# Kernel optimization log

Measured on AMD Instinct MI355X. Metric: run time of the kernel, lower is better.

## Reference

```python
import jax, jax.numpy as jnp
import numpy as np
from jax import lax

B, T = 16, 128
H, FD = 24, 4          # H hours, FD fourier harmonics
L = 64                 # latent_dim
D = 256                # d_model
NH = 8                 # heads
C = 1 + H * FD         # cont_dim = 97
EPS = 1e-5


def setup_inputs() -> dict:
    key = jax.random.key(0)
    ks = jax.random.split(key, 32)
    r = lambda k, sh, s: (jax.random.normal(k, sh, dtype=jnp.float32) * s)
    z = lambda sh: jnp.zeros(sh, dtype=jnp.float32)
    o = lambda sh: jnp.ones(sh, dtype=jnp.float32)
    return {
        'x_cont': jax.random.normal(ks[0], (B, T, C), dtype=jnp.float32),
        'z0': z((1, 1, L)),                       # learned initial hidden state
        'W_ih': r(ks[1], (L, 1), 0.1),            # RNN input weights
        'W_hh': r(ks[2], (L, L), 0.1),            # RNN recurrent weights
        'b_ih': z((L,)),
        'b_hh': z((L,)),
        'Uf': r(ks[3], (H, FD), 0.01),            # fourier coefficients
        'Wfp': r(ks[4], (L, H), 0.05),            # fourier_proj (L != H)
        'bfp': z((L,)),
        'feat_embed': r(ks[5], (L, D), 0.02),
        'W_in': r(ks[6], (3 * D, D), 0.02),       # MHA in_proj
        'b_in': z((3 * D,)),
        'W_ao': r(ks[7], (D, D), 0.02),           # MHA out_proj
        'b_ao': z((D,)),
        'g1': o((D,)), 'be1': z((D,)),            # ln1
        'W1': r(ks[8], (4 * D, D), 0.02), 'b1': z((4 * D,)),
        'W2': r(ks[9], (D, 4 * D), 0.02), 'b2': z((D,)),
        'g2': o((D,)), 'be2': z((D,)),            # ln2
        'Wop': r(ks[10], (1, D), 0.02), 'bop': z((1,)),   # out_proj d_model->1
        'Wg': r(ks[11], (L, L), 0.05), 'bg': z((L,)),     # gate
        'A': r(ks[12], (H, L), 0.01),
        'c': z((H,)),
    }


def _ln(x, g, b):
    mu = jnp.mean(x, -1, keepdims=True)
    var = jnp.mean(jnp.square(x - mu), -1, keepdims=True)
    return (x - mu) * lax.rsqrt(var + EPS) * g + b


def reference(x_cont, z0, W_ih, W_hh, b_ih, b_hh, Uf, Wfp, bfp, feat_embed,
              W_in, b_in, W_ao, b_ao, g1, be1, W1, b1, W2, b2, g2, be2,
              Wop, bop, Wg, bg, A, c):
    Bb, Tt, Cc = x_cont.shape
    x0 = x_cont[:, :, :1]              # (B,T,1)
    xf = x_cont[:, :, 1:]              # (B,T,H*FD)

    # --- single-layer relu RNN over time ---
    h0 = jnp.broadcast_to(z0[0, 0], (Bb, L))

    def step(h, x_t):                  # x_t: (B,1)
        h = jax.nn.relu(x_t @ W_ih.T + b_ih + h @ W_hh.T + b_hh)
        return h, h

    _, hs = lax.scan(step, h0, jnp.swapaxes(x0, 0, 1))
    h = jnp.swapaxes(hs, 0, 1)         # (B,T,L)

    # --- fourier features ---
    xf_mat = xf.reshape(Bb, Tt, H, FD)
    fourier_h = jnp.einsum('bthf,hf->bth', xf_mat, Uf)   # (B,T,H)
    z = h + fourier_h @ Wfp.T + bfp                      # (B,T,L)

    # --- feature attention: tokens (B*T, L, D) ---
    N = Bb * Tt
    zf = z.reshape(N, L)
    tokens = zf[:, :, None] * feat_embed[None]           # (N,L,D)

    qkv = tokens @ W_in.T + b_in                         # (N,L,3D)
    q, k, v = jnp.split(qkv, 3, axis=-1)
    dh = D // NH
    split_heads = lambda t: t.reshape(N, L, NH, dh).transpose(0, 2, 1, 3)
    q, k, v = split_heads(q), split_heads(k), split_heads(v)
    att = jax.nn.softmax(jnp.einsum('nhqd,nhkd->nhqk', q, k) / np.sqrt(dh), axis=-1)
    ao = jnp.einsum('nhqk,nhkd->nhqd', att, v).transpose(0, 2, 1, 3).reshape(N, L, D)
    ao = ao @ W_ao.T + b_ao

    t1 = _ln(tokens + ao, g1, be1)
    ffn = jax.nn.relu(t1 @ W1.T + b1) @ W2.T + b2
    t2 = _ln(t1 + ffn, g2, be2)
    delta = (t2 @ Wop.T + bop)[..., 0].reshape(Bb, Tt, L)

    gate = jax.nn.sigmoid(z @ Wg.T + bg)
    z_out = z + gate * delta

    o = z_out @ A.T + c                                  # (B,T,H)
    return (o, z_out)
```

## Files before the change

kernel.cpp:

```cpp
#include <hip/hip_runtime.h>

typedef short bf16x8 __attribute__((ext_vector_type(8)));
typedef float f32x4  __attribute__((ext_vector_type(4)));

__device__ __forceinline__ unsigned short f2b(float f){
  union { float f; unsigned u; } v; v.f = f;
  unsigned r = v.u + 0x7FFFu + ((v.u >> 16) & 1u);
  return (unsigned short)(r >> 16);
}
__device__ __forceinline__ float b2f(unsigned short s){
  union { unsigned u; float f; } v; v.u = ((unsigned)s) << 16;
  return v.f;
}
__device__ __forceinline__ unsigned pk2(float lo, float hi){
  unsigned r;
  asm("v_cvt_pk_bf16_f32 %0, %1, %2" : "=v"(r) : "v"(lo), "v"(hi));
  return r;
}

__global__ void k_pre_qkv(const float* __restrict__ FE, const float* __restrict__ W_in,
                          float* __restrict__ Qm, float* __restrict__ Km, float* __restrict__ Vm){
  int id = blockIdx.x*256 + threadIdx.x;
  int part = id >> 14;
  int l = (id >> 8) & 63;
  int d = id & 255;
  const float4* fe = (const float4*)(FE + l*256);
  const float4* wr = (const float4*)(W_in + (part*256 + d)*256);
  float s = 0.f;
  #pragma unroll 8
  for (int k=0;k<64;k++){
    float4 a = fe[k], b = wr[k];
    s += a.x*b.x + a.y*b.y + a.z*b.z + a.w*b.w;
  }
  float* dst = (part==0)?Qm:((part==1)?Km:Vm);
  dst[l*256+d] = s;
}

__global__ void k_pre2(const float* __restrict__ Qm, const float* __restrict__ Km,
                       const float* __restrict__ Vm,
                       const float* __restrict__ b_in, const float* __restrict__ W_ao,
                       const float* __restrict__ b_ao, const float* __restrict__ FE,
                       float* __restrict__ Gc, float* __restrict__ U,
                       float* __restrict__ W, float* __restrict__ S,
                       float* __restrict__ abias, short* __restrict__ M2c,
                       const float* __restrict__ W1, const float* __restrict__ W2,
                       short* __restrict__ W1c, short* __restrict__ W2c,
                       float* __restrict__ FEc,
                       const float* __restrict__ x_cont, const float* __restrict__ z0,
                       const float* __restrict__ W_ih, const float* __restrict__ W_hh,
                       const float* __restrict__ b_ih, const float* __restrict__ b_hh,
                       const float* __restrict__ Uf, const float* __restrict__ Wfp,
                       const float* __restrict__ bfp, float* __restrict__ zout){
  int bid = blockIdx.x;
  int tid = threadIdx.x;
  if (bid < 198){
    int id = bid*256 + tid;
    const float inv = 0.17677669529663687f;
    if (id < 32768){
      int h = id >> 12, ks = (id>>11)&1, w4 = (id>>9)&3, lane = (id>>3)&63, j = id&7;
      int lq = w4*16 + (lane&15);
      int lk = ks*32 + (lane>>4)*8 + j;
      const float* qp = Qm + lq*256 + h*32;
      const float* kp = Km + lk*256 + h*32;
      float s=0.f;
      #pragma unroll
      for (int d=0;d<32;d++) s += qp[d]*kp[d];
      Gc[id] = s*inv;
    } else if (id < 33280){
      int j = id - 32768; int h = j>>6, lq = j&63;
      const float* qp = Qm + lq*256 + h*32;
      const float* bk = b_in + 256 + h*32;
      float s=0.f;
      #pragma unroll
      for (int d=0;d<32;d++) s += qp[d]*bk[d];
      U[j] = s*inv;
    } else if (id < 33792){
      int j = id - 33280; int h = j>>6, lk = j&63;
      const float* kp = Km + lk*256 + h*32;
      const float* bq = b_in + h*32;
      float s=0.f;
      #pragma unroll
      for (int d=0;d<32;d++) s += bq[d]*kp[d];
      W[j] = s*inv;
    } else if (id < 33800){
      int h = id - 33792;
      float s=0.f;
      #pragma unroll
      for (int d=0;d<32;d++) s += b_in[h*32+d]*b_in[256+h*32+d];
      S[h] = s*inv;
    } else if (id < 34056){
      int e = id - 33800;
      float s = b_ao[e];
      for (int d=0; d<256; d++) s += b_in[512+d]*W_ao[e*256+d];
      abias[e] = s;
    } else if (id < 50440){
      int o = id - 34056;
      int tt = o>>12, et = (o>>10)&3, w4 = (o>>8)&3, lane = (o>>2)&63, j = o&3;
      int row = tt*16 + (lane&15);
      int col = w4*64 + et*16 + (lane>>4)*4 + j;
      FEc[o] = FE[row*256 + col];
    }
    return;
  }
  if (bid < 710){
    int o = (bid-198)*256 + tid;
    int h = o>>14, ks = (o>>13)&1, w4 = (o>>11)&3, et = (o>>9)&3, lane = (o>>3)&63, j = o&7;
    int e = w4*64 + et*16 + (lane&15);
    int lk = ks*32 + (lane>>4)*8 + j;
    const float* vp = Vm + lk*256 + h*32;
    const float* wp = W_ao + e*256 + h*32;
    float s=0.f;
    #pragma unroll
    for (int d=0;d<32;d++) s += vp[d]*wp[d];
    M2c[o] = (short)f2b(s);
    return;
  }
  if (bid < 2758){
    int id3 = (bid-710)*256 + tid;
    if (id3 < 262144){
      int o = id3;
      int c = o>>15, ks = (o>>12)&7, w4 = (o>>10)&3, ct = (o>>9)&1, lane = (o>>3)&63, j = o&7;
      int row = c*128 + w4*32 + ct*16 + (lane&15);
      int col = ks*32 + (lane>>4)*8 + j;
      W1c[o] = (short)f2b(W1[row*256 + col]);
    } else {
      int o = id3 - 262144;
      int c = o>>15, ks2 = (o>>13)&3, w4 = (o>>11)&3, et = (o>>9)&3, lane = (o>>3)&63, j = o&7;
      int row = w4*64 + et*16 + (lane&15);
      int col = c*128 + ks2*32 + (lane>>4)*8 + j;
      W2c[o] = (short)f2b(W2[row*1024 + col]);
    }
    return;
  }
  {
    int b = bid - 2758;
    int l = tid;
    bool act = (l < 64);
    __shared__ float h_sh[64];
    __shared__ float fh_sh[24];
    __shared__ float WfpT[24][64];
    float wr[64];
    float wih=0, bb=0, bf=0;
    float uf0=0,uf1=0,uf2=0,uf3=0;
    if (act){
      #pragma unroll
      for (int j=0;j<64;j++) wr[j] = W_hh[l*64+j];
      #pragma unroll
      for (int j=0;j<24;j++) WfpT[j][l] = Wfp[l*24+j];
      wih = W_ih[l];
      bb  = b_ih[l] + b_hh[l];
      bf  = bfp[l];
      if (l < 24){ uf0=Uf[l*4+0]; uf1=Uf[l*4+1]; uf2=Uf[l*4+2]; uf3=Uf[l*4+3]; }
      h_sh[l] = z0[l];
    }
    __syncthreads();
    const float* xb = x_cont + (size_t)b*128*97;
    for (int t=0;t<128;t++){
      float hn = 0.f, fh = 0.f;
      if (act){
        float x0 = xb[t*97];
        float a0=0,a1=0,a2=0,a3=0;
        #pragma unroll
        for (int j=0;j<64;j+=4){
          a0 += wr[j  ]*h_sh[j  ];
          a1 += wr[j+1]*h_sh[j+1];
          a2 += wr[j+2]*h_sh[j+2];
          a3 += wr[j+3]*h_sh[j+3];
        }
        hn = fmaxf(x0*wih + bb + ((a0+a1)+(a2+a3)), 0.f);
        if (l < 24){
          const float* xf = xb + t*97 + 1 + l*4;
          fh = xf[0]*uf0 + xf[1]*uf1 + xf[2]*uf2 + xf[3]*uf3;
        }
      }
      __syncthreads();
      if (act){
        h_sh[l] = hn;
        if (l < 24) fh_sh[l] = fh;
      }
      __syncthreads();
      if (act){
        float zv = hn + bf;
        #pragma unroll
        for (int j=0;j<24;j++) zv += fh_sh[j]*WfpT[j][l];
        zout[((size_t)b*128 + t)*64 + l] = zv;
      }
    }
  }
}

__global__ __launch_bounds__(256, 2) void k_main(
  const float* __restrict__ zall, const float* __restrict__ Gc,
  const float* __restrict__ Ubuf, const float* __restrict__ Wbuf, const float* __restrict__ Sbuf,
  const float* __restrict__ abias, const short* __restrict__ M2c,
  const float* __restrict__ FEc,
  const short* __restrict__ W1c, const float* __restrict__ b1,
  const short* __restrict__ W2c, const float* __restrict__ b2,
  const float* __restrict__ g1, const float* __restrict__ be1,
  const float* __restrict__ g2, const float* __restrict__ be2,
  const float* __restrict__ Wop, const float* __restrict__ bop,
  const float* __restrict__ Wg, const float* __restrict__ bg,
  const float* __restrict__ Amat, const float* __restrict__ cvec,
  float* __restrict__ out)
{
  const int n = blockIdx.x;
  const int tid = threadIdx.x;
  const int w = tid >> 6, lane = tid & 63, lg = lane >> 4, lr = lane & 15;
  const int cb = w * 64;

  __shared__ __align__(16) short t1_sh[64][264];
  __shared__ __align__(16) char  upoolA[17408];
  __shared__ __align__(16) char  upoolB[17408];
  __shared__ float redA[4][64];
  __shared__ float redB[4][64];
  __shared__ float z_sh[64];

  short (*midA)[136] = reinterpret_cast<short (*)[136]>(upoolA);
  short (*midB)[136] = reinterpret_cast<short (*)[136]>(upoolB);
  short (*pa_sh)[4][2][64][8] = reinterpret_cast<short (*)[4][2][64][8]>(upoolA);

  if (tid < 64) z_sh[tid] = zall[n*64 + tid];
  __syncthreads();

  float zkf[16];
  #pragma unroll
  for (int i=0;i<16;i++) zkf[i] = z_sh[(i>>3)*32 + lg*8 + (i&7)];

  f32x4 acc[4][4];
  #pragma unroll
  for (int et=0;et<4;et++)
    #pragma unroll
    for (int tt=0;tt<4;tt++){ f32x4 zz = {0.f,0.f,0.f,0.f}; acc[et][tt] = zz; }

  const int lq_own = w*16 + lr;
  const float zq_own = z_sh[lq_own];

  #pragma unroll 1
  for (int h=0; h<8; ++h){
    bf16x8 am[8];
    #pragma unroll
    for (int ks=0;ks<2;ks++)
      #pragma unroll
      for (int et=0;et<4;et++)
        am[ks*4+et] = *(const bf16x8*)(M2c + h*16384 + ks*8192 + w*2048 + et*512 + lane*8);
    {
      const float sh = Sbuf[h];
      const float uh = Ubuf[h*64 + lq_own];
      float e0[16];
      #pragma unroll
      for (int ks=0;ks<2;ks++){
        const float* gbase = Gc + h*4096 + ks*2048 + w*512 + lane*8;
        f32x4 ga = *(const f32x4*)(gbase);
        f32x4 gb = *(const f32x4*)(gbase + 4);
        f32x4 wa = *(const f32x4*)(Wbuf + h*64 + ks*32 + lg*8);
        f32x4 wb = *(const f32x4*)(Wbuf + h*64 + ks*32 + lg*8 + 4);
        #pragma unroll
        for (int j=0;j<4;j++){
          float zk = zkf[ks*8+j];
          e0[ks*8+j]   = zq_own*(zk*ga[j] + uh) + (zk*wa[j] + sh);
          float zk2 = zkf[ks*8+4+j];
          e0[ks*8+4+j] = zq_own*(zk2*gb[j] + uh) + (zk2*wb[j] + sh);
        }
      }
      float mx = e0[0];
      #pragma unroll
      for (int i=1;i<16;i++) mx = fmaxf(mx, e0[i]);
      mx = fmaxf(mx, __shfl_xor(mx,16));
      mx = fmaxf(mx, __shfl_xor(mx,32));
      float sum = 0.f;
      #pragma unroll
      for (int i=0;i<16;i++){ e0[i] = __expf(e0[i]-mx); sum += e0[i]; }
      sum += __shfl_xor(sum,16);
      sum += __shfl_xor(sum,32);
      float inv = 1.f/sum;
      #pragma unroll
      for (int ks=0;ks<2;ks++){
        union { bf16x8 v; unsigned u[4]; } pa;
        #pragma unroll
        for (int p=0;p<4;p++)
          pa.u[p] = pk2(e0[ks*8+2*p]*inv*zkf[ks*8+2*p], e0[ks*8+2*p+1]*inv*zkf[ks*8+2*p+1]);
        *(bf16x8*)&pa_sh[h&1][w][ks][lane][0] = pa.v;
      }
    }
    __syncthreads();
    __builtin_amdgcn_s_setprio(1);
    #pragma unroll
    for (int ks=0; ks<2; ks++){
      bf16x8 bt[4];
      #pragma unroll
      for (int tt=0;tt<4;tt++) bt[tt] = *(const bf16x8*)&pa_sh[h&1][tt][ks][lane][0];
      #pragma unroll
      for (int et=0;et<4;et++)
        #pragma unroll
        for (int tt=0;tt<4;tt++)
          acc[et][tt] = __builtin_amdgcn_mfma_f32_16x16x32_bf16(am[ks*4+et], bt[tt], acc[et][tt], 0,0,0);
    }
    __builtin_amdgcn_s_setprio(0);
  }

  f32x4 ab4[4], g14[4], be14[4];
  #pragma unroll
  for (int et=0;et<4;et++){
    int e0_ = cb + et*16 + lg*4;
    ab4[et]  = *(const f32x4*)(abias + e0_);
    g14[et]  = *(const f32x4*)(g1 + e0_);
    be14[et] = *(const f32x4*)(be1 + e0_);
  }
  float sum1[4], ssq1[4];
  #pragma unroll
  for (int tt=0;tt<4;tt++){
    int tok = tt*16 + lr;
    float zt = z_sh[tok];
    float s = 0.f, sq = 0.f;
    #pragma unroll
    for (int et=0;et<4;et++){
      f32x4 fe = *(const f32x4*)(FEc + tt*4096 + et*1024 + w*256 + lane*4);
      #pragma unroll
      for (int r=0;r<4;r++){
        float v = acc[et][tt][r] + ab4[et][r] + zt*fe[r];
        acc[et][tt][r] = v; s += v; sq += v*v;
      }
    }
    s  += __shfl_xor(s,16);  s  += __shfl_xor(s,32);
    sq += __shfl_xor(sq,16); sq += __shfl_xor(sq,32);
    sum1[tt] = s; ssq1[tt] = sq;
  }
  if (lane < 16){
    #pragma unroll
    for (int tt=0;tt<4;tt++){ redA[w][tt*16+lane] = sum1[tt]; redB[w][tt*16+lane] = ssq1[tt]; }
  }
  __syncthreads();
  float mu1[4], rs1[4];
  #pragma unroll
  for (int tt=0;tt<4;tt++){
    int tok = tt*16 + lr;
    float s  = redA[0][tok] + redA[1][tok] + redA[2][tok] + redA[3][tok];
    float sq = redB[0][tok] + redB[1][tok] + redB[2][tok] + redB[3][tok];
    float m = s * (1.f/256.f);
    mu1[tt] = m;
    rs1[tt] = rsqrtf(sq*(1.f/256.f) - m*m + 1e-5f);
  }
  #pragma unroll
  for (int et=0;et<4;et++)
    #pragma unroll
    for (int tt=0;tt<4;tt++){
      uint2 p;
      float v0 = (acc[et][tt][0]-mu1[tt])*rs1[tt]*g14[et][0] + be14[et][0];
      float v1 = (acc[et][tt][1]-mu1[tt])*rs1[tt]*g14[et][1] + be14[et][1];
      float v2 = (acc[et][tt][2]-mu1[tt])*rs1[tt]*g14[et][2] + be14[et][2];
      float v3 = (acc[et][tt][3]-mu1[tt])*rs1[tt]*g14[et][3] + be14[et][3];
      p.x = pk2(v0,v1); p.y = pk2(v2,v3);
      *(uint2*)&t1_sh[tt*16+lr][cb + et*16 + lg*4] = p;
    }
  __syncthreads();

  #pragma unroll
  for (int et=0;et<4;et++)
    #pragma unroll
    for (int tt=0;tt<4;tt++){ f32x4 zz = {0.f,0.f,0.f,0.f}; acc[et][tt] = zz; }

  #pragma unroll 1
  for (int c=0; c<8; c++){
    f32x4 midv[2][4];
    #pragma unroll
    for (int ct=0;ct<2;ct++){
      f32x4 bi = *(const f32x4*)(b1 + c*128 + w*32 + ct*16 + lg*4);
      #pragma unroll
      for (int tt=0;tt<4;tt++) midv[ct][tt] = bi;
    }
    bf16x8 aw2[16];
    #pragma unroll
    for (int ks2=0;ks2<2;ks2++)
      #pragma unroll
      for (int et=0;et<4;et++)
        aw2[ks2*4+et] = *(const bf16x8*)(W2c + c*32768 + ks2*8192 + w*2048 + et*512 + lane*8);
    #pragma unroll
    for (int ks=0; ks<4; ks++){
      bf16x8 bt[4], aw[2];
      #pragma unroll
      for (int tt=0;tt<4;tt++) bt[tt] = *(const bf16x8*)&t1_sh[tt*16+lr][ks*32 + lg*8];
      #pragma unroll
      for (int ct=0;ct<2;ct++)
        aw[ct] = *(const bf16x8*)(W1c + c*32768 + ks*4096 + w*1024 + ct*512 + lane*8);
      #pragma unroll
      for (int ct=0;ct<2;ct++)
        #pragma unroll
        for (int tt=0;tt<4;tt++)
          midv[ct][tt] = __builtin_amdgcn_mfma_f32_16x16x32_bf16(aw[ct], bt[tt], midv[ct][tt], 0,0,0);
    }
    #pragma unroll
    for (int ks2=2;ks2<4;ks2++)
      #pragma unroll
      for (int et=0;et<4;et++)
        aw2[ks2*4+et] = *(const bf16x8*)(W2c + c*32768 + ks2*8192 + w*2048 + et*512 + lane*8);
    #pragma unroll
    for (int ks=4; ks<8; ks++){
      bf16x8 bt[4], aw[2];
      #pragma unroll
      for (int tt=0;tt<4;tt++) bt[tt] = *(const bf16x8*)&t1_sh[tt*16+lr][ks*32 + lg*8];
      #pragma unroll
      for (int ct=0;ct<2;ct++)
        aw[ct] = *(const bf16x8*)(W1c + c*32768 + ks*4096 + w*1024 + ct*512 + lane*8);
      #pragma unroll
      for (int ct=0;ct<2;ct++)
        #pragma unroll
        for (int tt=0;tt<4;tt++)
          midv[ct][tt] = __builtin_amdgcn_mfma_f32_16x16x32_bf16(aw[ct], bt[tt], midv[ct][tt], 0,0,0);
    }
    short (*mids_)[136] = (c & 1) ? midB : midA;
    #pragma unroll
    for (int ct=0;ct<2;ct++)
      #pragma unroll
      for (int tt=0;tt<4;tt++){
        uint2 p;
        p.x = pk2(fmaxf(midv[ct][tt][0],0.f), fmaxf(midv[ct][tt][1],0.f));
        p.y = pk2(fmaxf(midv[ct][tt][2],0.f), fmaxf(midv[ct][tt][3],0.f));
        *(uint2*)&mids_[tt*16+lr][w*32 + ct*16 + lg*4] = p;
      }
    __syncthreads();
    __builtin_amdgcn_s_setprio(1);
    #pragma unroll
    for (int ks2=0; ks2<4; ks2++){
      bf16x8 bm[4];
      #pragma unroll
      for (int tt=0;tt<4;tt++) bm[tt] = *(const bf16x8*)&mids_[tt*16+lr][ks2*32 + lg*8];
      #pragma unroll
      for (int et=0;et<4;et++)
        #pragma unroll
        for (int tt=0;tt<4;tt++)
          acc[et][tt] = __builtin_amdgcn_mfma_f32_16x16x32_bf16(aw2[ks2*4+et], bm[tt], acc[et][tt], 0,0,0);
    }
    __builtin_amdgcn_s_setprio(0);
  }

  f32x4 b24[4], g24[4], be24[4], wop4[4];
  #pragma unroll
  for (int et=0;et<4;et++){
    int e0_ = cb + et*16 + lg*4;
    b24[et]  = *(const f32x4*)(b2 + e0_);
    g24[et]  = *(const f32x4*)(g2 + e0_);
    be24[et] = *(const f32x4*)(be2 + e0_);
    wop4[et] = *(const f32x4*)(Wop + e0_);
  }
  float sum2[4], ssq2[4];
  #pragma unroll
  for (int tt=0;tt<4;tt++){
    int tok = tt*16 + lr;
    float s = 0.f, sq = 0.f;
    #pragma unroll
    for (int et=0;et<4;et++){
      uint2 t1v = *(const uint2*)&t1_sh[tok][cb + et*16 + lg*4];
      #pragma unroll
      for (int r=0;r<4;r++){
        unsigned short hs = (unsigned short)((r&1) ? ((r<2?t1v.x:t1v.y)>>16) : ((r<2?t1v.x:t1v.y)&0xFFFF));
        float v = acc[et][tt][r] + b24[et][r] + b2f(hs);
        acc[et][tt][r] = v; s += v; sq += v*v;
      }
    }
    s  += __shfl_xor(s,16);  s  += __shfl_xor(s,32);
    sq += __shfl_xor(sq,16); sq += __shfl_xor(sq,32);
    sum2[tt] = s; ssq2[tt] = sq;
  }
  if (lane < 16){
    #pragma unroll
    for (int tt=0;tt<4;tt++){ redA[w][tt*16+lane] = sum2[tt]; redB[w][tt*16+lane] = ssq2[tt]; }
  }
  __syncthreads();

  float gate = 0.f;
  if (tid < 64){
    float gacc = bg[tid];
    const f32x4* wgr = (const f32x4*)(Wg + tid*64);
    #pragma unroll
    for (int j=0;j<16;j++){
      f32x4 wv = wgr[j];
      f32x4 zv = *(const f32x4*)(z_sh + j*4);
      gacc += wv[0]*zv[0] + wv[1]*zv[1] + wv[2]*zv[2] + wv[3]*zv[3];
    }
    gate = 1.f/(1.f + __expf(-gacc));
  }

  float dpart[4];
  #pragma unroll
  for (int tt=0;tt<4;tt++){
    int tok = tt*16 + lr;
    float s  = redA[0][tok] + redA[1][tok] + redA[2][tok] + redA[3][tok];
    float sq = redB[0][tok] + redB[1][tok] + redB[2][tok] + redB[3][tok];
    float m = s * (1.f/256.f);
    float rs = rsqrtf(sq*(1.f/256.f) - m*m + 1e-5f);
    float d = 0.f;
    #pragma unroll
    for (int et=0;et<4;et++)
      #pragma unroll
      for (int r=0;r<4;r++){
        float t2 = (acc[et][tt][r]-m)*rs*g24[et][r] + be24[et][r];
        d += t2*wop4[et][r];
      }
    d += __shfl_xor(d,16); d += __shfl_xor(d,32);
    dpart[tt] = d;
  }
  __syncthreads();
  if (lane < 16){
    #pragma unroll
    for (int tt=0;tt<4;tt++) redA[w][tt*16+lane] = dpart[tt];
  }
  __syncthreads();
  if (tid < 64){
    float delta = redA[0][tid]+redA[1][tid]+redA[2][tid]+redA[3][tid] + bop[0];
    float zo = z_sh[tid] + gate*delta;
    out[49152 + (size_t)n*64 + tid] = zo;
    z_sh[tid] = zo;
  }
  __syncthreads();
  if (tid < 24){
    const float* ar = Amat + tid*64;
    float s = cvec[tid];
    #pragma unroll
    for (int j=0;j<64;j++) s += z_sh[j]*ar[j];
    out[(size_t)n*24 + tid] = s;
  }
}

extern "C" void kernel_launch(void* const* d_in, const int* in_sizes, int n_in,
                              void* d_out, int out_size, void* d_ws, size_t ws_size,
                              hipStream_t stream) {
  const float* x_cont = (const float*)d_in[0];
  const float* z0    = (const float*)d_in[1];
  const float* W_ih  = (const float*)d_in[2];
  const float* W_hh  = (const float*)d_in[3];
  const float* b_ih  = (const float*)d_in[4];
  const float* b_hh  = (const float*)d_in[5];
  const float* Uf    = (const float*)d_in[6];
  const float* Wfp   = (const float*)d_in[7];
  const float* bfp   = (const float*)d_in[8];
  const float* FE    = (const float*)d_in[9];
  const float* W_in  = (const float*)d_in[10];
  const float* b_in  = (const float*)d_in[11];
  const float* W_ao  = (const float*)d_in[12];
  const float* b_ao  = (const float*)d_in[13];
  const float* g1    = (const float*)d_in[14];
  const float* be1   = (const float*)d_in[15];
  const float* W1    = (const float*)d_in[16];
  const float* b1    = (const float*)d_in[17];
  const float* W2    = (const float*)d_in[18];
  const float* b2    = (const float*)d_in[19];
  const float* g2    = (const float*)d_in[20];
  const float* be2   = (const float*)d_in[21];
  const float* Wop   = (const float*)d_in[22];
  const float* bop   = (const float*)d_in[23];
  const float* Wg    = (const float*)d_in[24];
  const float* bg    = (const float*)d_in[25];
  const float* Amat  = (const float*)d_in[26];
  const float* cvec  = (const float*)d_in[27];
  float* out = (float*)d_out;
  char* ws = (char*)d_ws;

  float* z    = (float*)(ws + 0);
  float* Qm   = (float*)(ws + 524288);
  float* Km   = (float*)(ws + 589824);
  float* Vm   = (float*)(ws + 655360);
  float* Gc   = (float*)(ws + 720896);
  float* U    = (float*)(ws + 851968);
  float* Wb   = (float*)(ws + 854016);
  float* S    = (float*)(ws + 856064);
  float* ab   = (float*)(ws + 856320);
  short* M2c  = (short*)(ws + 857344);
  short* W1c  = (short*)(ws + 1119488);
  short* W2c  = (short*)(ws + 1643776);
  float* FEc  = (float*)(ws + 2168064);

  hipLaunchKernelGGL(k_pre_qkv, dim3(192), dim3(256), 0, stream, FE, W_in, Qm, Km, Vm);
  hipLaunchKernelGGL(k_pre2, dim3(2774), dim3(256), 0, stream,
                     Qm, Km, Vm, b_in, W_ao, b_ao, FE, Gc, U, Wb, S, ab, M2c,
                     W1, W2, W1c, W2c, FEc,
                     x_cont, z0, W_ih, W_hh, b_ih, b_hh, Uf, Wfp, bfp, z);
  hipLaunchKernelGGL(k_main, dim3(2048), dim3(256), 0, stream, z, Gc, U, Wb, S, ab, M2c, FEc,
                     W1c, b1, W2c, b2, g1, be1, g2, be2, Wop, bop, Wg, bg, Amat, cvec, out);
}
```

Baseline: 336.6 us.

## Tile QKV precompute in shared memory, schedule RNN blocks first, coalesce weight reads

Rewrites the FE·W_inᵀ precompute as a shared-memory tiled GEMM in 12 blocks, with each thread accumulating 16 outputs instead of one thread per output doing a strided dot product. The sequential RNN blocks move to the front of the k_pre2 grid so the long serial recurrence starts first and can overlap the bulk work. The W1/W2 bf16 repack now reads source rows contiguously and scatters the writes, which coalesces the global loads. The tiled precompute uses only 12 blocks, which leaves most compute units idle during that kernel.

```diff
diff --git a/kernel.cpp b/kernel.cpp
--- a/kernel.cpp
+++ b/kernel.cpp
@@ -18,22 +18,36 @@
   return r;
 }
 
-__global__ void k_pre_qkv(const float* __restrict__ FE, const float* __restrict__ W_in,
+__global__ __launch_bounds__(256) void k_pre_qkv(const float* __restrict__ FE, const float* __restrict__ W_in,
                           float* __restrict__ Qm, float* __restrict__ Km, float* __restrict__ Vm){
-  int id = blockIdx.x*256 + threadIdx.x;
-  int part = id >> 14;
-  int l = (id >> 8) & 63;
-  int d = id & 255;
-  const float4* fe = (const float4*)(FE + l*256);
-  const float4* wr = (const float4*)(W_in + (part*256 + d)*256);
-  float s = 0.f;
-  #pragma unroll 8
-  for (int k=0;k<64;k++){
-    float4 a = fe[k], b = wr[k];
-    s += a.x*b.x + a.y*b.y + a.z*b.z + a.w*b.w;
+  const int part = blockIdx.x >> 2, db = blockIdx.x & 3;
+  const int tid = threadIdx.x;
+  const int l = tid & 63, dg = tid >> 6;
+  __shared__ float Wt[64][65];
+  __shared__ float Ft[64][65];
+  float acc[16];
+  #pragma unroll
+  for (int i=0;i<16;i++) acc[i]=0.f;
+  for (int kc=0;kc<4;kc++){
+    __syncthreads();
+    #pragma unroll
+    for (int t=0;t<16;t++){
+      int id = tid + t*256;
+      int r = id >> 6, kk = id & 63;
+      Wt[r][kk] = W_in[(size_t)(part*256 + db*64 + r)*256 + kc*64 + kk];
+      Ft[r][kk] = FE[(size_t)r*256 + kc*64 + kk];
+    }
+    __syncthreads();
+    #pragma unroll 8
+    for (int kk=0;kk<64;kk++){
+      float fv = Ft[l][kk];
+      #pragma unroll
+      for (int i=0;i<16;i++) acc[i] += fv * Wt[dg*16+i][kk];
+    }
   }
   float* dst = (part==0)?Qm:((part==1)?Km:Vm);
-  dst[l*256+d] = s;
+  #pragma unroll
+  for (int i=0;i<16;i++) dst[l*256 + db*64 + dg*16 + i] = acc[i];
 }
 
 __global__ void k_pre2(const float* __restrict__ Qm, const float* __restrict__ Km,
@@ -53,8 +67,64 @@
                        const float* __restrict__ bfp, float* __restrict__ zout){
   int bid = blockIdx.x;
   int tid = threadIdx.x;
-  if (bid < 198){
-    int id = bid*256 + tid;
+  if (bid < 16){
+    int b = bid;
+    int l = tid;
+    bool act = (l < 64);
+    __shared__ float h_sh[64];
+    __shared__ float fh_sh[24];
+    __shared__ float WfpT[24][64];
+    float wr[64];
+    float wih=0, bb=0, bf=0;
+    float uf0=0,uf1=0,uf2=0,uf3=0;
+    if (act){
+      #pragma unroll
+      for (int j=0;j<64;j++) wr[j] = W_hh[l*64+j];
+      #pragma unroll
+      for (int j=0;j<24;j++) WfpT[j][l] = Wfp[l*24+j];
+      wih = W_ih[l];
+      bb  = b_ih[l] + b_hh[l];
+      bf  = bfp[l];
+      if (l < 24){ uf0=Uf[l*4+0]; uf1=Uf[l*4+1]; uf2=Uf[l*4+2]; uf3=Uf[l*4+3]; }
+      h_sh[l] = z0[l];
+    }
+    __syncthreads();
+    const float* xb = x_cont + (size_t)b*128*97;
+    for (int t=0;t<128;t++){
+      float hn = 0.f, fh = 0.f;
+      if (act){
+        float x0 = xb[t*97];
+        float a0=0,a1=0,a2=0,a3=0;
+        #pragma unroll
+        for (int j=0;j<64;j+=4){
+          a0 += wr[j  ]*h_sh[j  ];
+          a1 += wr[j+1]*h_sh[j+1];
+          a2 += wr[j+2]*h_sh[j+2];
+          a3 += wr[j+3]*h_sh[j+3];
+        }
+        hn = fmaxf(x0*wih + bb + ((a0+a1)+(a2+a3)), 0.f);
+        if (l < 24){
+          const float* xf = xb + t*97 + 1 + l*4;
+          fh = xf[0]*uf0 + xf[1]*uf1 + xf[2]*uf2 + xf[3]*uf3;
+        }
+      }
+      __syncthreads();
+      if (act){
+        h_sh[l] = hn;
+        if (l < 24) fh_sh[l] = fh;
+      }
+      __syncthreads();
+      if (act){
+        float zv = hn + bf;
+        #pragma unroll
+        for (int j=0;j<24;j++) zv += fh_sh[j]*WfpT[j][l];
+        zout[((size_t)b*128 + t)*64 + l] = zv;
+      }
+    }
+    return;
+  }
+  if (bid < 214){
+    int id = (bid-16)*256 + tid;
     const float inv = 0.17677669529663687f;
     if (id < 32768){
       int h = id >> 12, ks = (id>>11)&1, w4 = (id>>9)&3, lane = (id>>3)&63, j = id&7;
@@ -102,8 +172,8 @@
     }
     return;
   }
-  if (bid < 710){
-    int o = (bid-198)*256 + tid;
+  if (bid < 726){
+    int o = (bid-214)*256 + tid;
     int h = o>>14, ks = (o>>13)&1, w4 = (o>>11)&3, et = (o>>9)&3, lane = (o>>3)&63, j = o&7;
     int e = w4*64 + et*16 + (lane&15);
     int lk = ks*32 + (lane>>4)*8 + j;
@@ -115,77 +185,23 @@
     M2c[o] = (short)f2b(s);
     return;
   }
-  if (bid < 2758){
-    int id3 = (bid-710)*256 + tid;
+  {
+    int id3 = (bid-726)*256 + tid;
     if (id3 < 262144){
-      int o = id3;
-      int c = o>>15, ks = (o>>12)&7, w4 = (o>>10)&3, ct = (o>>9)&1, lane = (o>>3)&63, j = o&7;
-      int row = c*128 + w4*32 + ct*16 + (lane&15);
-      int col = ks*32 + (lane>>4)*8 + j;
-      W1c[o] = (short)f2b(W1[row*256 + col]);
+      int row = id3 >> 8, col = id3 & 255;
+      int c = row >> 7, w4 = (row>>5)&3, ct = (row>>4)&1, lrow = row & 15;
+      int ks = col >> 5, lhi = (col>>3)&3, j = col & 7;
+      int o = c*32768 + ks*4096 + w4*1024 + ct*512 + (lhi*16+lrow)*8 + j;
+      W1c[o] = (short)f2b(W1[id3]);
     } else {
-      int o = id3 - 262144;
-      int c = o>>15, ks2 = (o>>13)&3, w4 = (o>>11)&3, et = (o>>9)&3, lane = (o>>3)&63, j = o&7;
-      int row = w4*64 + et*16 + (lane&15);
-      int col = c*128 + ks2*32 + (lane>>4)*8 + j;
-      W2c[o] = (short)f2b(W2[row*1024 + col]);
+      int idx = id3 - 262144;
+      int row = idx >> 10, col = idx & 1023;
+      int w4 = row >> 6, et = (row>>4)&3, lrow = row & 15;
+      int c = col >> 7, ks2 = (col>>5)&3, lhi = (col>>3)&3, j = col & 7;
+      int o = c*32768 + ks2*8192 + w4*2048 + et*512 + (lhi*16+lrow)*8 + j;
+      W2c[o] = (short)f2b(W2[idx]);
     }
     return;
-  }
-  {
-    int b = bid - 2758;
-    int l = tid;
-    bool act = (l < 64);
-    __shared__ float h_sh[64];
-    __shared__ float fh_sh[24];
-    __shared__ float WfpT[24][64];
-    float wr[64];
-    float wih=0, bb=0, bf=0;
-    float uf0=0,uf1=0,uf2=0,uf3=0;
-    if (act){
-      #pragma unroll
-      for (int j=0;j<64;j++) wr[j] = W_hh[l*64+j];
-      #pragma unroll
-      for (int j=0;j<24;j++) WfpT[j][l] = Wfp[l*24+j];
-      wih = W_ih[l];
-      bb  = b_ih[l] + b_hh[l];
-      bf  = bfp[l];
-      if (l < 24){ uf0=Uf[l*4+0]; uf1=Uf[l*4+1]; uf2=Uf[l*4+2]; uf3=Uf[l*4+3]; }
-      h_sh[l] = z0[l];
-    }
-    __syncthreads();
-    const float* xb = x_cont + (size_t)b*128*97;
-    for (int t=0;t<128;t++){
-      float hn = 0.f, fh = 0.f;
-      if (act){
-        float x0 = xb[t*97];
-        float a0=0,a1=0,a2=0,a3=0;
-        #pragma unroll
-        for (int j=0;j<64;j+=4){
-          a0 += wr[j  ]*h_sh[j  ];
-          a1 += wr[j+1]*h_sh[j+1];
-          a2 += wr[j+2]*h_sh[j+2];
-          a3 += wr[j+3]*h_sh[j+3];
-        }
-        hn = fmaxf(x0*wih + bb + ((a0+a1)+(a2+a3)), 0.f);
-        if (l < 24){
-          const float* xf = xb + t*97 + 1 + l*4;
-          fh = xf[0]*uf0 + xf[1]*uf1 + xf[2]*uf2 + xf[3]*uf3;
-        }
-      }
-      __syncthreads();
-      if (act){
-        h_sh[l] = hn;
-        if (l < 24) fh_sh[l] = fh;
-      }
-      __syncthreads();
-      if (act){
-        float zv = hn + bf;
-        #pragma unroll
-        for (int j=0;j<24;j++) zv += fh_sh[j]*WfpT[j][l];
-        zout[((size_t)b*128 + t)*64 + l] = zv;
-      }
-    }
   }
 }
 
@@ -569,7 +585,7 @@
   short* W2c  = (short*)(ws + 1643776);
   float* FEc  = (float*)(ws + 2168064);
 
-  hipLaunchKernelGGL(k_pre_qkv, dim3(192), dim3(256), 0, stream, FE, W_in, Qm, Km, Vm);
+  hipLaunchKernelGGL(k_pre_qkv, dim3(12), dim3(256), 0, stream, FE, W_in, Qm, Km, Vm);
   hipLaunchKernelGGL(k_pre2, dim3(2774), dim3(256), 0, stream,
                      Qm, Km, Vm, b_in, W_ao, b_ao, FE, Gc, U, Wb, S, ab, M2c,
                      W1, W2, W1c, W2c, FEc,
```

Result: slower. 358.4 us (+6.5%).

## Raise k_main occupancy to three blocks, move RNN blocks first, coalesce weight repack

Applied to the files above, without the earlier changes.

k_main's launch bounds go from two to three blocks per CU. To fit, the double-buffered FFN mid buffer becomes a single buffer guarded by an extra barrier, and the M2c/W2 fragments are loaded just before use instead of prefetched into registers. In the prep kernel, the serial RNN blocks now take the lowest block indices so they start first, and the W1/W2 bf16 repack reads its source coalesced and scatters the writes. The trade is less latency hiding and an extra sync per chunk in exchange for more resident waves.

```diff
diff --git a/kernel.cpp b/kernel.cpp
--- a/kernel.cpp
+++ b/kernel.cpp
@@ -53,8 +53,64 @@
                        const float* __restrict__ bfp, float* __restrict__ zout){
   int bid = blockIdx.x;
   int tid = threadIdx.x;
-  if (bid < 198){
-    int id = bid*256 + tid;
+  if (bid < 16){
+    int b = bid;
+    int l = tid;
+    bool act = (l < 64);
+    __shared__ float h_sh[64];
+    __shared__ float fh_sh[24];
+    __shared__ float WfpT[24][64];
+    float wr[64];
+    float wih=0, bb=0, bf=0;
+    float uf0=0,uf1=0,uf2=0,uf3=0;
+    if (act){
+      #pragma unroll
+      for (int j=0;j<64;j++) wr[j] = W_hh[l*64+j];
+      #pragma unroll
+      for (int j=0;j<24;j++) WfpT[j][l] = Wfp[l*24+j];
+      wih = W_ih[l];
+      bb  = b_ih[l] + b_hh[l];
+      bf  = bfp[l];
+      if (l < 24){ uf0=Uf[l*4+0]; uf1=Uf[l*4+1]; uf2=Uf[l*4+2]; uf3=Uf[l*4+3]; }
+      h_sh[l] = z0[l];
+    }
+    __syncthreads();
+    const float* xb = x_cont + (size_t)b*128*97;
+    for (int t=0;t<128;t++){
+      float hn = 0.f, fh = 0.f;
+      if (act){
+        float x0 = xb[t*97];
+        float a0=0,a1=0,a2=0,a3=0;
+        #pragma unroll
+        for (int j=0;j<64;j+=4){
+          a0 += wr[j  ]*h_sh[j  ];
+          a1 += wr[j+1]*h_sh[j+1];
+          a2 += wr[j+2]*h_sh[j+2];
+          a3 += wr[j+3]*h_sh[j+3];
+        }
+        hn = fmaxf(x0*wih + bb + ((a0+a1)+(a2+a3)), 0.f);
+        if (l < 24){
+          const float* xf = xb + t*97 + 1 + l*4;
+          fh = xf[0]*uf0 + xf[1]*uf1 + xf[2]*uf2 + xf[3]*uf3;
+        }
+      }
+      __syncthreads();
+      if (act){
+        h_sh[l] = hn;
+        if (l < 24) fh_sh[l] = fh;
+      }
+      __syncthreads();
+      if (act){
+        float zv = hn + bf;
+        #pragma unroll
+        for (int j=0;j<24;j++) zv += fh_sh[j]*WfpT[j][l];
+        zout[((size_t)b*128 + t)*64 + l] = zv;
+      }
+    }
+    return;
+  }
+  if (bid < 214){
+    int id = (bid-16)*256 + tid;
     const float inv = 0.17677669529663687f;
     if (id < 32768){
       int h = id >> 12, ks = (id>>11)&1, w4 = (id>>9)&3, lane = (id>>3)&63, j = id&7;
@@ -102,8 +158,8 @@
     }
     return;
   }
-  if (bid < 710){
-    int o = (bid-198)*256 + tid;
+  if (bid < 726){
+    int o = (bid-214)*256 + tid;
     int h = o>>14, ks = (o>>13)&1, w4 = (o>>11)&3, et = (o>>9)&3, lane = (o>>3)&63, j = o&7;
     int e = w4*64 + et*16 + (lane&15);
     int lk = ks*32 + (lane>>4)*8 + j;
@@ -115,81 +171,27 @@
     M2c[o] = (short)f2b(s);
     return;
   }
-  if (bid < 2758){
-    int id3 = (bid-710)*256 + tid;
+  {
+    int id3 = (bid-726)*256 + tid;
     if (id3 < 262144){
-      int o = id3;
-      int c = o>>15, ks = (o>>12)&7, w4 = (o>>10)&3, ct = (o>>9)&1, lane = (o>>3)&63, j = o&7;
-      int row = c*128 + w4*32 + ct*16 + (lane&15);
-      int col = ks*32 + (lane>>4)*8 + j;
-      W1c[o] = (short)f2b(W1[row*256 + col]);
+      int row = id3 >> 8, col = id3 & 255;
+      int c = row >> 7, w4 = (row>>5)&3, ct = (row>>4)&1, lrow = row & 15;
+      int ks = col >> 5, lhi = (col>>3)&3, j = col & 7;
+      int o = c*32768 + ks*4096 + w4*1024 + ct*512 + (lhi*16+lrow)*8 + j;
+      W1c[o] = (short)f2b(W1[id3]);
     } else {
-      int o = id3 - 262144;
-      int c = o>>15, ks2 = (o>>13)&3, w4 = (o>>11)&3, et = (o>>9)&3, lane = (o>>3)&63, j = o&7;
-      int row = w4*64 + et*16 + (lane&15);
-      int col = c*128 + ks2*32 + (lane>>4)*8 + j;
-      W2c[o] = (short)f2b(W2[row*1024 + col]);
+      int idx = id3 - 262144;
+      int row = idx >> 10, col = idx & 1023;
+      int w4 = row >> 6, et = (row>>4)&3, lrow = row & 15;
+      int c = col >> 7, ks2 = (col>>5)&3, lhi = (col>>3)&3, j = col & 7;
+      int o = c*32768 + ks2*8192 + w4*2048 + et*512 + (lhi*16+lrow)*8 + j;
+      W2c[o] = (short)f2b(W2[idx]);
     }
     return;
   }
-  {
-    int b = bid - 2758;
-    int l = tid;
-    bool act = (l < 64);
-    __shared__ float h_sh[64];
-    __shared__ float fh_sh[24];
-    __shared__ float WfpT[24][64];
-    float wr[64];
-    float wih=0, bb=0, bf=0;
-    float uf0=0,uf1=0,uf2=0,uf3=0;
-    if (act){
-      #pragma unroll
-      for (int j=0;j<64;j++) wr[j] = W_hh[l*64+j];
-      #pragma unroll
-      for (int j=0;j<24;j++) WfpT[j][l] = Wfp[l*24+j];
-      wih = W_ih[l];
-      bb  = b_ih[l] + b_hh[l];
-      bf  = bfp[l];
-      if (l < 24){ uf0=Uf[l*4+0]; uf1=Uf[l*4+1]; uf2=Uf[l*4+2]; uf3=Uf[l*4+3]; }
-      h_sh[l] = z0[l];
-    }
-    __syncthreads();
-    const float* xb = x_cont + (size_t)b*128*97;
-    for (int t=0;t<128;t++){
-      float hn = 0.f, fh = 0.f;
-      if (act){
-        float x0 = xb[t*97];
-        float a0=0,a1=0,a2=0,a3=0;
-        #pragma unroll
-        for (int j=0;j<64;j+=4){
-          a0 += wr[j  ]*h_sh[j  ];
-          a1 += wr[j+1]*h_sh[j+1];
-          a2 += wr[j+2]*h_sh[j+2];
-          a3 += wr[j+3]*h_sh[j+3];
-        }
-        hn = fmaxf(x0*wih + bb + ((a0+a1)+(a2+a3)), 0.f);
-        if (l < 24){
-          const float* xf = xb + t*97 + 1 + l*4;
-          fh = xf[0]*uf0 + xf[1]*uf1 + xf[2]*uf2 + xf[3]*uf3;
-        }
-      }
-      __syncthreads();
-      if (act){
-        h_sh[l] = hn;
-        if (l < 24) fh_sh[l] = fh;
-      }
-      __syncthreads();
-      if (act){
-        float zv = hn + bf;
-        #pragma unroll
-        for (int j=0;j<24;j++) zv += fh_sh[j]*WfpT[j][l];
-        zout[((size_t)b*128 + t)*64 + l] = zv;
-      }
-    }
-  }
-}
-
-__global__ __launch_bounds__(256, 2) void k_main(
+}
+
+__global__ __launch_bounds__(256, 3) void k_main(
   const float* __restrict__ zall, const float* __restrict__ Gc,
   const float* __restrict__ Ubuf, const float* __restrict__ Wbuf, const float* __restrict__ Sbuf,
   const float* __restrict__ abias, const short* __restrict__ M2c,
@@ -209,15 +211,13 @@
   const int cb = w * 64;
 
   __shared__ __align__(16) short t1_sh[64][264];
-  __shared__ __align__(16) char  upoolA[17408];
-  __shared__ __align__(16) char  upoolB[17408];
+  __shared__ __align__(16) char  upool[17408];
   __shared__ float redA[4][64];
   __shared__ float redB[4][64];
   __shared__ float z_sh[64];
 
-  short (*midA)[136] = reinterpret_cast<short (*)[136]>(upoolA);
-  short (*midB)[136] = reinterpret_cast<short (*)[136]>(upoolB);
-  short (*pa_sh)[4][2][64][8] = reinterpret_cast<short (*)[4][2][64][8]>(upoolA);
+  short (*mid_sh)[136] = reinterpret_cast<short (*)[136]>(upool);
+  short (*pa_sh)[4][2][64][8] = reinterpret_cast<short (*)[4][2][64][8]>(upool);
 
   if (tid < 64) z_sh[tid] = zall[n*64 + tid];
   __syncthreads();
@@ -237,12 +237,6 @@
 
   #pragma unroll 1
   for (int h=0; h<8; ++h){
-    bf16x8 am[8];
-    #pragma unroll
-    for (int ks=0;ks<2;ks++)
-      #pragma unroll
-      for (int et=0;et<4;et++)
-        am[ks*4+et] = *(const bf16x8*)(M2c + h*16384 + ks*8192 + w*2048 + et*512 + lane*8);
     {
       const float sh = Sbuf[h];
       const float uh = Ubuf[h*64 + lq_own];
@@ -286,14 +280,17 @@
     __builtin_amdgcn_s_setprio(1);
     #pragma unroll
     for (int ks=0; ks<2; ks++){
-      bf16x8 bt[4];
+      bf16x8 am[4], bt[4];
+      #pragma unroll
+      for (int et=0;et<4;et++)
+        am[et] = *(const bf16x8*)(M2c + h*16384 + ks*8192 + w*2048 + et*512 + lane*8);
       #pragma unroll
       for (int tt=0;tt<4;tt++) bt[tt] = *(const bf16x8*)&pa_sh[h&1][tt][ks][lane][0];
       #pragma unroll
       for (int et=0;et<4;et++)
         #pragma unroll
         for (int tt=0;tt<4;tt++)
-          acc[et][tt] = __builtin_amdgcn_mfma_f32_16x16x32_bf16(am[ks*4+et], bt[tt], acc[et][tt], 0,0,0);
+          acc[et][tt] = __builtin_amdgcn_mfma_f32_16x16x32_bf16(am[et], bt[tt], acc[et][tt], 0,0,0);
     }
     __builtin_amdgcn_s_setprio(0);
   }
@@ -368,14 +365,8 @@
       #pragma unroll
       for (int tt=0;tt<4;tt++) midv[ct][tt] = bi;
     }
-    bf16x8 aw2[16];
-    #pragma unroll
-    for (int ks2=0;ks2<2;ks2++)
-      #pragma unroll
-      for (int et=0;et<4;et++)
-        aw2[ks2*4+et] = *(const bf16x8*)(W2c + c*32768 + ks2*8192 + w*2048 + et*512 + lane*8);
-    #pragma unroll
-    for (int ks=0; ks<4; ks++){
+    #pragma unroll
+    for (int ks=0; ks<8; ks++){
       bf16x8 bt[4], aw[2];
       #pragma unroll
       for (int tt=0;tt<4;tt++) bt[tt] = *(const bf16x8*)&t1_sh[tt*16+lr][ks*32 + lg*8];
@@ -388,26 +379,7 @@
         for (int tt=0;tt<4;tt++)
           midv[ct][tt] = __builtin_amdgcn_mfma_f32_16x16x32_bf16(aw[ct], bt[tt], midv[ct][tt], 0,0,0);
     }
-    #pragma unroll
-    for (int ks2=2;ks2<4;ks2++)
-      #pragma unroll
-      for (int et=0;et<4;et++)
-        aw2[ks2*4+et] = *(const bf16x8*)(W2c + c*32768 + ks2*8192 + w*2048 + et*512 + lane*8);
-    #pragma unroll
-    for (int ks=4; ks<8; ks++){
-      bf16x8 bt[4], aw[2];
-      #pragma unroll
-      for (int tt=0;tt<4;tt++) bt[tt] = *(const bf16x8*)&t1_sh[tt*16+lr][ks*32 + lg*8];
-      #pragma unroll
-      for (int ct=0;ct<2;ct++)
-        aw[ct] = *(const bf16x8*)(W1c + c*32768 + ks*4096 + w*1024 + ct*512 + lane*8);
-      #pragma unroll
-      for (int ct=0;ct<2;ct++)
-        #pragma unroll
-        for (int tt=0;tt<4;tt++)
-          midv[ct][tt] = __builtin_amdgcn_mfma_f32_16x16x32_bf16(aw[ct], bt[tt], midv[ct][tt], 0,0,0);
-    }
-    short (*mids_)[136] = (c & 1) ? midB : midA;
+    __syncthreads();
     #pragma unroll
     for (int ct=0;ct<2;ct++)
       #pragma unroll
@@ -415,20 +387,23 @@
         uint2 p;
         p.x = pk2(fmaxf(midv[ct][tt][0],0.f), fmaxf(midv[ct][tt][1],0.f));
         p.y = pk2(fmaxf(midv[ct][tt][2],0.f), fmaxf(midv[ct][tt][3],0.f));
-        *(uint2*)&mids_[tt*16+lr][w*32 + ct*16 + lg*4] = p;
+        *(uint2*)&mid_sh[tt*16+lr][w*32 + ct*16 + lg*4] = p;
       }
     __syncthreads();
     __builtin_amdgcn_s_setprio(1);
     #pragma unroll
     for (int ks2=0; ks2<4; ks2++){
-      bf16x8 bm[4];
-      #pragma unroll
-      for (int tt=0;tt<4;tt++) bm[tt] = *(const bf16x8*)&mids_[tt*16+lr][ks2*32 + lg*8];
+      bf16x8 aw2[4], bm[4];
       #pragma unroll
       for (int et=0;et<4;et++)
+        aw2[et] = *(const bf16x8*)(W2c + c*32768 + ks2*8192 + w*2048 + et*512 + lane*8);
+      #pragma unroll
+      for (int tt=0;tt<4;tt++) bm[tt] = *(const bf16x8*)&mid_sh[tt*16+lr][ks2*32 + lg*8];
+      #pragma unroll
+      for (int et=0;et<4;et++)
         #pragma unroll
         for (int tt=0;tt<4;tt++)
-          acc[et][tt] = __builtin_amdgcn_mfma_f32_16x16x32_bf16(aw2[ks2*4+et], bm[tt], acc[et][tt], 0,0,0);
+          acc[et][tt] = __builtin_amdgcn_mfma_f32_16x16x32_bf16(aw2[et], bm[tt], acc[et][tt], 0,0,0);
     }
     __builtin_amdgcn_s_setprio(0);
   }
```

After: 335.4 us. Within noise of the previous version (-0.4%).
